# Performance work log

Measured on AMD Instinct MI355X. Metric: run time of the kernel, lower is better.

Reference implementation:

```python
import jax, jax.numpy as jnp
import numpy as np

NCLASSES = 21
CONF_THRESH = 0.5
IOU_THRESH = 0.45
TOP_K = 200
NMS_MAX_OUT = 400
NEG = jnp.float32(-1e9)  # sentinel for suppressed / below-threshold scores

B, N_BOXES = 8, 8732
LAST = NCLASSES + 4 * (NCLASSES - 1) + 1  # 102


def setup_inputs() -> dict:
    key = jax.random.key(0)
    kc, kxy, kwh, ke = jax.random.split(key, 4)
    conf = jax.random.uniform(kc, (B, N_BOXES, NCLASSES), dtype=jnp.float32)
    # plausible normalized boxes: xmin,ymin in [0,0.8], width/height in [0.01,0.2]
    xy = jax.random.uniform(kxy, (B, N_BOXES, NCLASSES - 1, 2), minval=0.0, maxval=0.8)
    wh = jax.random.uniform(kwh, (B, N_BOXES, NCLASSES - 1, 2), minval=0.01, maxval=0.2)
    boxes = jnp.concatenate([xy, xy + wh], axis=-1).reshape(B, N_BOXES, 4 * (NCLASSES - 1))
    extra = jax.random.uniform(ke, (B, N_BOXES, 1), dtype=jnp.float32)
    y_pred = jnp.concatenate([conf, boxes, extra], axis=-1)  # [B, N, 102]
    return {"y_pred": y_pred}


def _iou_one_vs_all(box, boxes):
    # box: [4] (xmin,ymin,xmax,ymax); boxes: [N,4]
    x1 = jnp.maximum(box[0], boxes[:, 0])
    y1 = jnp.maximum(box[1], boxes[:, 1])
    x2 = jnp.minimum(box[2], boxes[:, 2])
    y2 = jnp.minimum(box[3], boxes[:, 3])
    inter = jnp.maximum(x2 - x1, 0.0) * jnp.maximum(y2 - y1, 0.0)
    area_a = (box[2] - box[0]) * (box[3] - box[1])
    area_b = (boxes[:, 2] - boxes[:, 0]) * (boxes[:, 3] - boxes[:, 1])
    union = area_a + area_b - inter
    return jnp.where(union > 0.0, inter / union, 0.0)


def _nms_one_class(rows):
    # rows: [N, 7] = (class_id, conf, xmin, ymin, xmax, ymax, extra)
    n = rows.shape[0]
    scores0 = jnp.where(rows[:, 1] > CONF_THRESH, rows[:, 1], NEG)
    boxes = rows[:, 2:6]
    idx_range = jnp.arange(n)

    def step(live, _):
        best = jnp.argmax(live)
        valid = live[best] > NEG * 0.5  # any real score passed the threshold
        ious = _iou_one_vs_all(boxes[best], boxes)
        suppress = valid & ((ious > IOU_THRESH) | (idx_range == best))
        live = jnp.where(suppress, NEG, live)
        return live, (best, valid)

    _, (sel, selv) = jax.lax.scan(step, scores0, None, length=NMS_MAX_OUT)
    # gather selected rows; zero-pad invalid slots (matches tf.pad with 0)
    out = jnp.where(selv[:, None], rows[sel], 0.0)  # [NMS_MAX_OUT, 7]
    return out


def _per_image(item):
    # item: [N, 102]
    n = item.shape[0]
    conf = item[:, 1:NCLASSES]                                  # [N, C-1]
    boxes = item[:, NCLASSES:NCLASSES + 4 * (NCLASSES - 1)].reshape(n, NCLASSES - 1, 4)
    extra = item[:, -1]                                         # [N]
    class_ids = jnp.arange(1, NCLASSES, dtype=item.dtype)       # [C-1]
    rows = jnp.concatenate([
        jnp.broadcast_to(class_ids[:, None, None], (NCLASSES - 1, n, 1)),
        conf.T[:, :, None],
        jnp.transpose(boxes, (1, 0, 2)),
        jnp.broadcast_to(extra[None, :, None], (NCLASSES - 1, n, 1)),
    ], axis=-1)                                                 # [C-1, N, 7]
    per_class = jax.vmap(_nms_one_class)(rows)                  # [C-1, MAX_OUT, 7]
    filtered = per_class.reshape(-1, 7)                         # [(C-1)*MAX_OUT, 7]
    _, top_idx = jax.lax.top_k(filtered[:, 1], TOP_K)           # sorted descending
    return filtered[top_idx]                                    # [TOP_K, 7]


def reference(y_pred):
    return jax.vmap(_per_image)(y_pred)  # [B, TOP_K, 7]
```

## Files before the change

kernel.cpp:

```cpp
#include <hip/hip_runtime.h>
#include <cstdint>

#define NB 8
#define NBOX 8732
#define NCL 21
#define NCM1 20
#define LASTD 102
#define CONF_TH 0.5f
#define IOU_TH 0.45f
#define TOPK 200
#define MAXOUT 400
#define SELCAP 200
#define EMITN 256
#define NTASK (NB * NCM1)
#define THREADS 1024
#define NW 16
#define NIT 9
#define NBIN 2048
#define KPAD 8768
#define NBATCH (KPAD / 64)
#define NTR 1024
#define KPAD_TR (NTR + 64)
#define NBATCH_TR (KPAD_TR / 64)
#define CPAD 8736

#define MIDD ((double)IOU_TH + 0x1p-26)


struct SM {
    float4 selbox[SELCAP];
    float selA[SELCAP];
    uint64_t selkey[SELCAP];
    uint64_t keys[KPAD];
    uint64_t smask[2][64];
    unsigned long long extC[2];
    int hist[NBIN];
    int binstart[NBIN];
    int wavetot[NW];
    int Mshare, MtrShare, nselshare, prevNshare, doneflag;
};

__device__ __forceinline__ int iou_sup(float4 a, float aA, float4 b, float bA) {
    float x1 = fmaxf(a.x, b.x), y1 = fmaxf(a.y, b.y);
    float x2 = fminf(a.z, b.z), y2 = fminf(a.w, b.w);
    float iw = fmaxf(__fsub_rn(x2, x1), 0.0f);
    float ih = fmaxf(__fsub_rn(y2, y1), 0.0f);
    float inter = __fmul_rn(iw, ih);
    float uni = __fsub_rn(__fadd_rn(aA, bA), inter);
    return (double)inter > MIDD * (double)uni;
}

__device__ __forceinline__ float4 load_box(const float* __restrict__ img,
                                           int boxoff, uint64_t key) {
    if ((key >> 32) == 0) return make_float4(0.f, 0.f, 0.f, 0.f);
    uint32_t i = 0xFFFFFFFFu - (uint32_t)key;
    const float* bp = img + (size_t)i * LASTD + boxoff;
    return make_float4(bp[0], bp[1], bp[2], bp[3]);
}

__device__ __forceinline__ float box_area(float4 b) {
    return __fmul_rn(__fsub_rn(b.z, b.x), __fsub_rn(b.w, b.y));
}

__device__ __forceinline__ float4 shfl_box(float4 b, int c) {
    float4 r;
    r.x = __shfl(b.x, c); r.y = __shfl(b.y, c);
    r.z = __shfl(b.z, c); r.w = __shfl(b.w, c);
    return r;
}

__device__ __forceinline__ uint64_t shfl_xor_u64(uint64_t v, int m) {
    return (uint64_t)__shfl_xor((unsigned long long)v, m, 64);
}

__global__ __launch_bounds__(256) void transpose_conf(const float* __restrict__ yp,
                                                      float* __restrict__ confT,
                                                      float* __restrict__ extraT) {
    const uint32_t TOT4 = (uint32_t)NB * NBOX * LASTD / 4u;
    for (uint32_t i4 = blockIdx.x * blockDim.x + threadIdx.x; i4 < TOT4;
         i4 += gridDim.x * blockDim.x) {
        float4 v = ((const float4*)yp)[i4];
        uint32_t base = i4 * 4u;
        #pragma unroll
        for (int k = 0; k < 4; ++k) {
            uint32_t flat = base + k;
            uint32_t b = flat / (NBOX * LASTD);
            uint32_t rem = flat - b * (NBOX * LASTD);
            uint32_t row = rem / LASTD;
            uint32_t col = rem - row * LASTD;
            float f = (k == 0) ? v.x : (k == 1) ? v.y : (k == 2) ? v.z : v.w;
            if (col - 1u < (uint32_t)NCM1)
                confT[((size_t)b * NCM1 + (col - 1u)) * CPAD + row] = f;
            else if (col == LASTD - 1)
                extraT[(size_t)b * CPAD + row] = f;
        }
    }
}

template <bool TRM>
__device__ void build_keys_impl(const float* __restrict__ confsrc, int cstride,
                                SM& sm, int tid, int lane, int wav,
                                int& M, int& Mtr) {
    constexpr int PADT = TRM ? KPAD_TR : KPAD;
    float confs[NIT];
    #pragma unroll
    for (int it = 0; it < NIT; ++it) {
        int idx = it * THREADS + tid;
        confs[it] = (idx < NBOX) ? confsrc[(size_t)idx * cstride] : 0.0f;
    }
    sm.hist[tid] = 0; sm.hist[tid + THREADS] = 0;
    if (tid == 0) sm.MtrShare = 0;
    __syncthreads();

    #pragma unroll
    for (int it = 0; it < NIT; ++it) {
        int idx = it * THREADS + tid;
        if (idx < NBOX && confs[it] > CONF_TH) {
            int bin = (int)((__float_as_uint(confs[it]) - 0x3F000000u) >> 12);
            atomicAdd(&sm.hist[bin], 1);
        }
    }
    __syncthreads();

    int h0 = sm.hist[2 * tid], h1 = sm.hist[2 * tid + 1];
    int x = h0 + h1;
    int s = x;
    #pragma unroll
    for (int d = 1; d <= 32; d <<= 1) {
        int y = __shfl_down(s, d);
        if (lane + d < 64) s += y;
    }
    if (lane == 0) sm.wavetot[wav] = s;
    __syncthreads();
    int cross = 0;
    #pragma unroll
    for (int w = 0; w < NW; ++w)
        if (w > wav) cross += sm.wavetot[w];
    int Safter = cross + s - x;
    sm.binstart[2 * tid + 1] = Safter;
    sm.binstart[2 * tid] = Safter + h1;
    if (tid == 0) sm.Mshare = cross + s;
    if (TRM) {
        int cand = 0;
        if (Safter < NTR && h1 > 0) cand = Safter + h1;
        int bs0 = Safter + h1;
        if (bs0 < NTR && h0 > 0) { int c2 = bs0 + h0; cand = cand > c2 ? cand : c2; }
        if (cand > 0) atomicMax(&sm.MtrShare, cand);
    }
    sm.hist[2 * tid] = 0; sm.hist[2 * tid + 1] = 0;
    __syncthreads();
    M = sm.Mshare;
    Mtr = TRM ? sm.MtrShare : M;

    #pragma unroll
    for (int it = 0; it < NIT; ++it) {
        int idx = it * THREADS + tid;
        if (idx < NBOX && confs[it] > CONF_TH) {
            uint32_t bits = __float_as_uint(confs[it]);
            int bin = (int)((bits - 0x3F000000u) >> 12);
            if (!TRM || sm.binstart[bin] < NTR) {
                int slot = sm.binstart[bin] + atomicAdd(&sm.hist[bin], 1);
                if (!TRM || slot < PADT)
                    sm.keys[slot] = ((uint64_t)bits << 32) |
                                    (uint32_t)(0xFFFFFFFFu - (uint32_t)idx);
            }
        }
    }
    __syncthreads();
    int Mp = Mtr < PADT ? Mtr : PADT;
    for (int m = Mp + tid; m < PADT; m += THREADS) sm.keys[m] = 0;
    for (int f = tid; f < NBIN; f += THREADS) {
        int s0 = sm.binstart[f], h = sm.hist[f];
        if (TRM && (s0 >= NTR || s0 + h > PADT)) continue;
        for (int i2 = 1; i2 < h; ++i2) {
            uint64_t key = sm.keys[s0 + i2];
            int j = i2 - 1;
            while (j >= 0 && sm.keys[s0 + j] < key) {
                sm.keys[s0 + j + 1] = sm.keys[s0 + j];
                --j;
            }
            sm.keys[s0 + j + 1] = key;
        }
    }
    __syncthreads();
}

template <int KPADT, int NBATCHT>
__device__ int greedy_scan(const float* __restrict__ img, int boxoff, SM& sm,
                           int tid, int lane, int wav) {
    uint64_t keyC = sm.keys[lane];
    uint64_t keyN = sm.keys[64 + lane];
    float4 boxC = load_box(img, boxoff, keyC);
    float4 boxN = load_box(img, boxoff, keyN);
    float aC = box_area(boxC), aN = box_area(boxN);
    #pragma unroll
    for (int tt = 0; tt < 4; ++tt) {
        int c = wav + tt * NW;
        float4 cb = shfl_box(boxC, c);
        float ca = __shfl(aC, c);
        uint64_t row = 0;
        if (ca > 0.0f)
            row = __ballot(lane < c && iou_sup(cb, ca, boxC, aC));
        if (lane == 0) sm.smask[0][c] = row;
    }
    if (tid == 0) { sm.extC[0] = 0ull; sm.extC[1] = 0ull; }
    __syncthreads();

    int nsel = 0, prevN = 0;
    bool done = false;
    for (int i = 0; i < NBATCHT && !done; ++i) {
        const int p = i & 1;
        const bool vC = (keyC >> 32) != 0;
        {
            int sup = 0;
            for (int j = prevN + wav; j < nsel; j += NW)
                sup |= iou_sup(boxC, aC, sm.selbox[j], sm.selA[j]);
            unsigned long long bal = __ballot(vC && sup);
            if (lane == 0 && bal) atomicOr(&sm.extC[p], bal);
        }
        int f0 = (i + 2) * 64;
        uint64_t key2 = (f0 < KPADT) ? sm.keys[f0 + lane] : 0;
        float4 box2 = load_box(img, boxoff, key2);
        float a2 = box_area(box2);
        __syncthreads();
        const int nselPre = nsel;
        if (wav == 0) {
            unsigned long long V = __ballot(vC);
            unsigned long long E = sm.extC[p];
            if (lane == 0) sm.extC[p] = 0ull;
            uint64_t smc = sm.smask[p][lane];
            uint64_t alive = ~(E | ~V);
            uint64_t accm = 0;
            int cnt = nsel;
            while (alive && cnt < SELCAP) {
                int t = __ffsll((unsigned long long)alive) - 1;
                uint64_t bit = 1ull << t;
                accm |= bit;
                cnt++;
                unsigned long long kill = __ballot((smc >> t) & 1ull);
                alive &= ~(kill | bit);
            }
            if ((accm >> lane) & 1ull) {
                int pos = nsel + __popcll(accm & ((1ull << lane) - 1ull));
                sm.selbox[pos] = boxC;
                sm.selA[pos] = aC;
                sm.selkey[pos] = keyC;
            }
            if (lane == 0) {
                sm.nselshare = cnt;
                sm.prevNshare = nsel;
                sm.doneflag = (cnt >= SELCAP) || (V != ~0ull);
            }
        } else {
            float4 cb[5];
            float ca[5];
            unsigned amask = 0;
            #pragma unroll
            for (int k = 0; k < 5; ++k) {
                int c = (wav - 1) + k * (NW - 1);
                float4 t4 = make_float4(0.f, 0.f, 0.f, 0.f);
                float tA = 0.0f;
                if (c < 64) {
                    t4 = shfl_box(boxN, c);
                    tA = __shfl(aN, c);
                }
                cb[k] = t4; ca[k] = tA;
                if (c < 64 && tA > 0.0f) amask |= 1u << k;
            }
            unsigned long long sb = 0;
            for (int j0 = 0; j0 < nselPre && amask; j0 += 64) {
                int j = j0 + lane;
                bool jv = j < nselPre;
                float4 sbx = sm.selbox[jv ? j : 0];
                float sA = sm.selA[jv ? j : 0];
                #pragma unroll
                for (int k = 0; k < 5; ++k) {
                    if (!((amask >> k) & 1u)) continue;
                    int hit = jv && iou_sup(cb[k], ca[k], sbx, sA);
                    if (__ballot(hit)) {
                        amask &= ~(1u << k);
                        sb |= 1ull << ((wav - 1) + k * (NW - 1));
                    }
                }
            }
            #pragma unroll
            for (int k = 0; k < 5; ++k) {
                if (!((amask >> k) & 1u)) continue;
                int c = (wav - 1) + k * (NW - 1);
                uint64_t row = __ballot(lane < c && iou_sup(cb[k], ca[k], boxN, aN));
                if (lane == 0) sm.smask[p ^ 1][c] = row;
            }
            if (lane == 0 && sb) atomicOr(&sm.extC[p ^ 1], sb);
        }
        __syncthreads();
        nsel = sm.nselshare;
        prevN = sm.prevNshare;
        done = sm.doneflag != 0;
        keyC = keyN; boxC = boxN; aC = aN;
        keyN = key2; boxN = box2; aN = a2;
    }
    return nsel;
}

__device__ void emit_rows(const float* __restrict__ extrasrc, int estride,
                          int cm1, SM& sm, int nsel, float* __restrict__ rows,
                          int task, int tid) {
    float* out0 = rows + (size_t)task * MAXOUT * 7;
    for (int r = tid; r < EMITN; r += THREADS) {
        float* o = out0 + (size_t)r * 7;
        if (r < nsel) {
            uint64_t key = sm.selkey[r];
            uint32_t i = 0xFFFFFFFFu - (uint32_t)key;
            float4 bx = sm.selbox[r];
            o[0] = (float)(cm1 + 1);
            o[1] = __uint_as_float((uint32_t)(key >> 32));
            o[2] = bx.x;
            o[3] = bx.y;
            o[4] = bx.z;
            o[5] = bx.w;
            o[6] = extrasrc[(size_t)i * estride];
        } else {
            #pragma unroll
            for (int q = 0; q < 7; ++q) o[q] = 0.0f;
        }
    }
}

__global__ __launch_bounds__(THREADS) void nms_fast(const float* __restrict__ yp,
                                                    const float* __restrict__ confT,
                                                    const float* __restrict__ extraT,
                                                    float* __restrict__ rows) {
    __shared__ SM sm;
    const int task = blockIdx.x;
    const int b = task / NCM1;
    const int cm1 = task % NCM1;
    const int tid = threadIdx.x;
    const int lane = tid & 63;
    const int wav = tid >> 6;
    const float* img = yp + (size_t)b * NBOX * LASTD;
    const float* conf = confT + (size_t)task * CPAD;
    const int boxoff = NCL + 4 * cm1;

    int M, Mtr;
    build_keys_impl<true>(conf, 1, sm, tid, lane, wav, M, Mtr);
    int nsel = -1;
    if (Mtr <= KPAD_TR) {
        nsel = greedy_scan<KPAD_TR, NBATCH_TR>(img, boxoff, sm, tid, lane, wav);
        if (nsel < SELCAP && Mtr < M) nsel = -1;
    }
    if (nsel < 0) {
        build_keys_impl<false>(conf, 1, sm, tid, lane, wav, M, Mtr);
        nsel = greedy_scan<KPAD, NBATCH>(img, boxoff, sm, tid, lane, wav);
    }
    emit_rows(extraT + (size_t)b * CPAD, 1, cm1, sm, nsel, rows, task, tid);
}

__global__ __launch_bounds__(THREADS) void nms_mono(const float* __restrict__ yp,
                                                    float* __restrict__ rows) {
    __shared__ SM sm;
    const int task = blockIdx.x;
    const int b = task / NCM1;
    const int cm1 = task % NCM1;
    const int tid = threadIdx.x;
    const float* img = yp + (size_t)b * NBOX * LASTD;
    int M, Mtr;
    build_keys_impl<false>(img + 1 + cm1, LASTD, sm, tid, tid & 63, tid >> 6,
                           M, Mtr);
    int nsel = greedy_scan<KPAD, NBATCH>(img, NCL + 4 * cm1, sm, tid,
                                         tid & 63, tid >> 6);
    emit_rows(img + (LASTD - 1), LASTD, cm1, sm, nsel, rows, task, tid);
}

__global__ __launch_bounds__(THREADS) void topk_per_image(const float* __restrict__ rows,
                                                          float* __restrict__ out) {
    __shared__ uint64_t K[8192];
    const int b = blockIdx.x;
    const int tid = threadIdx.x;
    const float* rb = rows + (size_t)b * (NCM1 * MAXOUT) * 7;

    for (int xx = tid; xx < 8192; xx += THREADS) {
        int list = xx >> 8, r = xx & 255;
        uint64_t k = 0;
        if (list < NCM1) {
            int flat = list * MAXOUT + r;
            float conf = rb[(size_t)flat * 7 + 1];
            k = ((uint64_t)__float_as_uint(conf) << 32) |
                (uint32_t)(0xFFFFFFFFu - (uint32_t)flat);
        }
        K[xx] = k;
    }
    __syncthreads();

    for (int round = 0; round < 5; ++round) {
        int npairs = 16 >> round;
        int sep = 256 << round;
        for (int w = tid; w < npairs * 256; w += THREADS) {
            int p = w >> 8, t = w & 255;
            int A = p * 2 * sep;
            uint64_t a = K[A + t];
            uint64_t c = K[A + sep + 255 - t];
            K[A + t] = a > c ? a : c;
        }
        __syncthreads();
        for (int j = 128; j >= 64; j >>= 1) {
            for (int w = tid; w < npairs * 128; w += THREADS) {
                int p = w >> 7, q = w & 127;
                int t = ((q & ~(j - 1)) << 1) | (q & (j - 1));
                int A = p * 2 * sep;
                uint64_t x0 = K[A + t];
                uint64_t x1 = K[A + t + j];
                if (x0 < x1) { K[A + t] = x1; K[A + t + j] = x0; }
            }
            __syncthreads();
        }
        for (int w = tid; w < npairs * 256; w += THREADS) {
            int p = w >> 8, t = w & 255;
            int xI = p * 2 * sep + t;
            uint64_t v = K[xI];
            #pragma unroll
            for (int j = 32; j >= 1; j >>= 1) {
                uint64_t pr = shfl_xor_u64(v, j);
                uint64_t mx = v > pr ? v : pr;
                uint64_t mn = v > pr ? pr : v;
                v = ((t & j) == 0) ? mx : mn;
            }
            K[xI] = v;
        }
        __syncthreads();
    }

    if (tid < TOPK) {
        uint64_t key = K[tid];
        uint32_t flat = 0xFFFFFFFFu - (uint32_t)key;
        const float* src = rb + (size_t)flat * 7;
        float* o = out + ((size_t)b * TOPK + tid) * 7;
        #pragma unroll
        for (int q = 0; q < 7; ++q) o[q] = src[q];
    }
}

extern "C" void kernel_launch(void* const* d_in, const int* in_sizes, int n_in,
                              void* d_out, int out_size, void* d_ws, size_t ws_size,
                              hipStream_t stream) {
    const float* yp = (const float*)d_in[0];
    float* rows = (float*)d_ws;
    const size_t rowsB = (size_t)NTASK * MAXOUT * 7 * sizeof(float);
    float* confT = (float*)((char*)d_ws + rowsB);
    const size_t confB = (size_t)NTASK * CPAD * sizeof(float);
    float* extraT = (float*)((char*)confT + confB);
    const size_t extraB = (size_t)NB * CPAD * sizeof(float);
    const size_t need = rowsB + confB + extraB;
    float* out = (float*)d_out;

    if (ws_size >= need) {
        hipLaunchKernelGGL(transpose_conf, dim3(2048), dim3(256), 0, stream,
                           yp, confT, extraT);
        hipLaunchKernelGGL(nms_fast, dim3(NTASK), dim3(THREADS), 0, stream,
                           yp, confT, extraT, rows);
    } else {
        hipLaunchKernelGGL(nms_mono, dim3(NTASK), dim3(THREADS), 0, stream,
                           yp, rows);
    }
    hipLaunchKernelGGL(topk_per_image, dim3(NB), dim3(THREADS), 0, stream,
                       rows, out);
}
```

Measured before the change: 59.34 us.

## Replace truncated greedy NMS scan with precomputed suppression bitmask matrix

The fast path now keeps only the top ~512-576 candidates. It precomputes a pairwise IoU suppression bitmask matrix in shared memory, built with wave ballots, and then runs the greedy selection as a single-wave bitmask sweep. This replaces the previous batched greedy scan over up to 1088 keys. The aim is to cut serialized per-selection IoU work and block-wide syncs. In exchange it uses a smaller truncation window, which may send more tasks down the full fallback path, and it spends extra shared memory on a union layout.

```diff
diff --git a/kernel.cpp b/kernel.cpp
--- a/kernel.cpp
+++ b/kernel.cpp
@@ -19,9 +19,9 @@
 #define NBIN 2048
 #define KPAD 8768
 #define NBATCH (KPAD / 64)
-#define NTR 1024
-#define KPAD_TR (NTR + 64)
-#define NBATCH_TR (KPAD_TR / 64)
+#define NTR 512
+#define NMX 576
+#define NWORD 9
 #define CPAD 8736
 
 #define MIDD ((double)IOU_TH + 0x1p-26)
@@ -38,6 +38,18 @@
     int binstart[NBIN];
     int wavetot[NW];
     int Mshare, MtrShare, nselshare, prevNshare, doneflag;
+};
+
+struct FastSM {
+    uint64_t keys[NMX];
+    uint64_t M[NMX][NWORD];
+    float4 bx[NMX];
+    float ar[NMX];
+    int acc[SELCAP];
+    int hist[NBIN];
+    int binstart[NBIN];
+    int wavetot[NW];
+    int Mshare, MtrShare, nselshare;
 };
 
 __device__ __forceinline__ int iou_sup(float4 a, float aA, float4 b, float bA) {
@@ -97,11 +109,10 @@
     }
 }
 
-template <bool TRM>
+template <class SMT, bool TRM, int PADT, int NTRT>
 __device__ void build_keys_impl(const float* __restrict__ confsrc, int cstride,
-                                SM& sm, int tid, int lane, int wav,
+                                SMT& sm, int tid, int lane, int wav,
                                 int& M, int& Mtr) {
-    constexpr int PADT = TRM ? KPAD_TR : KPAD;
     float confs[NIT];
     #pragma unroll
     for (int it = 0; it < NIT; ++it) {
@@ -142,9 +153,9 @@
     if (tid == 0) sm.Mshare = cross + s;
     if (TRM) {
         int cand = 0;
-        if (Safter < NTR && h1 > 0) cand = Safter + h1;
+        if (Safter < NTRT && h1 > 0) cand = Safter + h1;
         int bs0 = Safter + h1;
-        if (bs0 < NTR && h0 > 0) { int c2 = bs0 + h0; cand = cand > c2 ? cand : c2; }
+        if (bs0 < NTRT && h0 > 0) { int c2 = bs0 + h0; cand = cand > c2 ? cand : c2; }
         if (cand > 0) atomicMax(&sm.MtrShare, cand);
     }
     sm.hist[2 * tid] = 0; sm.hist[2 * tid + 1] = 0;
@@ -158,7 +169,7 @@
         if (idx < NBOX && confs[it] > CONF_TH) {
             uint32_t bits = __float_as_uint(confs[it]);
             int bin = (int)((bits - 0x3F000000u) >> 12);
-            if (!TRM || sm.binstart[bin] < NTR) {
+            if (!TRM || sm.binstart[bin] < NTRT) {
                 int slot = sm.binstart[bin] + atomicAdd(&sm.hist[bin], 1);
                 if (!TRM || slot < PADT)
                     sm.keys[slot] = ((uint64_t)bits << 32) |
@@ -171,7 +182,7 @@
     for (int m = Mp + tid; m < PADT; m += THREADS) sm.keys[m] = 0;
     for (int f = tid; f < NBIN; f += THREADS) {
         int s0 = sm.binstart[f], h = sm.hist[f];
-        if (TRM && (s0 >= NTR || s0 + h > PADT)) continue;
+        if (TRM && (s0 >= NTRT || s0 + h > PADT)) continue;
         for (int i2 = 1; i2 < h; ++i2) {
             uint64_t key = sm.keys[s0 + i2];
             int j = i2 - 1;
@@ -330,7 +341,7 @@
                                                     const float* __restrict__ confT,
                                                     const float* __restrict__ extraT,
                                                     float* __restrict__ rows) {
-    __shared__ SM sm;
+    __shared__ union USM { SM full; FastSM fast; } u;
     const int task = blockIdx.x;
     const int b = task / NCM1;
     const int cm1 = task % NCM1;
@@ -342,17 +353,93 @@
     const int boxoff = NCL + 4 * cm1;
 
     int M, Mtr;
-    build_keys_impl<true>(conf, 1, sm, tid, lane, wav, M, Mtr);
+    build_keys_impl<FastSM, true, NMX, NTR>(conf, 1, u.fast, tid, lane, wav,
+                                            M, Mtr);
     int nsel = -1;
-    if (Mtr <= KPAD_TR) {
-        nsel = greedy_scan<KPAD_TR, NBATCH_TR>(img, boxoff, sm, tid, lane, wav);
+    if (Mtr <= NMX) {
+        for (int c = tid; c < NMX; c += THREADS) {
+            float4 bb = load_box(img, boxoff, u.fast.keys[c]);
+            u.fast.bx[c] = bb;
+            u.fast.ar[c] = box_area(bb);
+        }
+        __syncthreads();
+        for (int k = 0; k < NMX / NW; ++k) {
+            int a = wav + k * NW;
+            float4 ab = u.fast.bx[a];
+            float aa = u.fast.ar[a];
+            if (aa > 0.0f) {
+                for (int w = a >> 6; w < NWORD; ++w) {
+                    int bc = w * 64 + lane;
+                    int hit = (bc > a) &&
+                              iou_sup(ab, aa, u.fast.bx[bc], u.fast.ar[bc]);
+                    unsigned long long bal = __ballot(hit);
+                    if (lane == 0) u.fast.M[a][w] = bal;
+                }
+            } else {
+                for (int w = a >> 6; w < NWORD; ++w)
+                    if (lane == 0) u.fast.M[a][w] = 0ull;
+            }
+        }
+        __syncthreads();
+        if (wav == 0) {
+            uint64_t alive = 0;
+            if (lane < NWORD) {
+                int rem = Mtr - lane * 64;
+                alive = (rem >= 64) ? ~0ull
+                      : (rem > 0 ? ((1ull << rem) - 1ull) : 0ull);
+            }
+            int cnt = 0;
+            for (int w = 0; w < NWORD && cnt < SELCAP; ++w) {
+                uint64_t cur = (uint64_t)__shfl((unsigned long long)alive, w);
+                while (cur && cnt < SELCAP) {
+                    int t = __ffsll((unsigned long long)cur) - 1;
+                    int c = w * 64 + t;
+                    if (lane == 0) u.fast.acc[cnt] = c;
+                    cnt++;
+                    uint64_t row = (lane < NWORD) ? u.fast.M[c][lane] : 0ull;
+                    alive &= ~row;
+                    uint64_t roww = (uint64_t)__shfl((unsigned long long)row, w);
+                    cur &= ~(roww | (1ull << t));
+                }
+            }
+            if (lane == 0) u.fast.nselshare = cnt;
+        }
+        __syncthreads();
+        nsel = u.fast.nselshare;
         if (nsel < SELCAP && Mtr < M) nsel = -1;
+        if (nsel >= 0) {
+            const float* extrasrc = extraT + (size_t)b * CPAD;
+            float* out0 = rows + (size_t)task * MAXOUT * 7;
+            for (int r = tid; r < EMITN; r += THREADS) {
+                float* o = out0 + (size_t)r * 7;
+                if (r < nsel) {
+                    int c = u.fast.acc[r];
+                    uint64_t key = u.fast.keys[c];
+                    uint32_t i = 0xFFFFFFFFu - (uint32_t)key;
+                    float4 bxv = u.fast.bx[c];
+                    o[0] = (float)(cm1 + 1);
+                    o[1] = __uint_as_float((uint32_t)(key >> 32));
+                    o[2] = bxv.x;
+                    o[3] = bxv.y;
+                    o[4] = bxv.z;
+                    o[5] = bxv.w;
+                    o[6] = extrasrc[i];
+                } else {
+                    #pragma unroll
+                    for (int q = 0; q < 7; ++q) o[q] = 0.0f;
+                }
+            }
+        }
     }
     if (nsel < 0) {
-        build_keys_impl<false>(conf, 1, sm, tid, lane, wav, M, Mtr);
-        nsel = greedy_scan<KPAD, NBATCH>(img, boxoff, sm, tid, lane, wav);
-    }
-    emit_rows(extraT + (size_t)b * CPAD, 1, cm1, sm, nsel, rows, task, tid);
+        __syncthreads();
+        int M2, Mt2;
+        build_keys_impl<SM, false, KPAD, 0>(conf, 1, u.full, tid, lane, wav,
+                                            M2, Mt2);
+        int ns2 = greedy_scan<KPAD, NBATCH>(img, boxoff, u.full, tid, lane, wav);
+        emit_rows(extraT + (size_t)b * CPAD, 1, cm1, u.full, ns2, rows, task,
+                  tid);
+    }
 }
 
 __global__ __launch_bounds__(THREADS) void nms_mono(const float* __restrict__ yp,
@@ -364,8 +451,8 @@
     const int tid = threadIdx.x;
     const float* img = yp + (size_t)b * NBOX * LASTD;
     int M, Mtr;
-    build_keys_impl<false>(img + 1 + cm1, LASTD, sm, tid, tid & 63, tid >> 6,
-                           M, Mtr);
+    build_keys_impl<SM, false, KPAD, 0>(img + 1 + cm1, LASTD, sm, tid,
+                                        tid & 63, tid >> 6, M, Mtr);
     int nsel = greedy_scan<KPAD, NBATCH>(img, NCL + 4 * cm1, sm, tid,
                                          tid & 63, tid >> 6);
     emit_rows(img + (LASTD - 1), LASTD, cm1, sm, nsel, rows, task, tid);
```

Measured after the change: 103.5 us. 1.74x slower.

## Stage conf transpose through shared-memory tiles and shrink NTR candidate threshold

Applied to the files above, without the earlier changes.

The conf/extra transpose now works in 64-row tiles per block. Each block stages the needed columns in LDS and then writes confT and extraT coalesced along the row dimension, replacing the scattered strided global stores. Separately, NTR drops from 1024 to 512 and KPAD_TR is padded by 128 instead of 64, which changes the truncated-candidate path of NMS. The retuned NTR may raise fallback frequency if more candidates are needed.

```diff
diff --git a/kernel.cpp b/kernel.cpp
--- a/kernel.cpp
+++ b/kernel.cpp
@@ -19,10 +19,14 @@
 #define NBIN 2048
 #define KPAD 8768
 #define NBATCH (KPAD / 64)
-#define NTR 1024
-#define KPAD_TR (NTR + 64)
+#define NTR 512
+#define KPAD_TR (NTR + 128)
 #define NBATCH_TR (KPAD_TR / 64)
 #define CPAD 8736
+#define TROWS 64
+#define NTILE ((NBOX + TROWS - 1) / TROWS)
+#define TSLOT 21
+#define TPITCH 68
 
 #define MIDD ((double)IOU_TH + 0x1p-26)
 
@@ -76,23 +80,41 @@
 __global__ __launch_bounds__(256) void transpose_conf(const float* __restrict__ yp,
                                                       float* __restrict__ confT,
                                                       float* __restrict__ extraT) {
-    const uint32_t TOT4 = (uint32_t)NB * NBOX * LASTD / 4u;
-    for (uint32_t i4 = blockIdx.x * blockDim.x + threadIdx.x; i4 < TOT4;
-         i4 += gridDim.x * blockDim.x) {
-        float4 v = ((const float4*)yp)[i4];
-        uint32_t base = i4 * 4u;
+    __shared__ float tile[TSLOT * TPITCH];
+    const int blk = blockIdx.x;
+    const int b = blk / NTILE;
+    const int t0 = blk - b * NTILE;
+    const int r0 = t0 * TROWS;
+    const int nrow = (NBOX - r0) < TROWS ? (NBOX - r0) : TROWS;
+    const int nflat4 = nrow * LASTD / 4;
+    const float4* src = (const float4*)(yp + ((size_t)b * NBOX + r0) * LASTD);
+
+    for (int i4 = threadIdx.x; i4 < nflat4; i4 += 256) {
+        float4 v = src[i4];
+        int base = i4 * 4;
         #pragma unroll
         for (int k = 0; k < 4; ++k) {
-            uint32_t flat = base + k;
-            uint32_t b = flat / (NBOX * LASTD);
-            uint32_t rem = flat - b * (NBOX * LASTD);
-            uint32_t row = rem / LASTD;
-            uint32_t col = rem - row * LASTD;
-            float f = (k == 0) ? v.x : (k == 1) ? v.y : (k == 2) ? v.z : v.w;
-            if (col - 1u < (uint32_t)NCM1)
-                confT[((size_t)b * NCM1 + (col - 1u)) * CPAD + row] = f;
-            else if (col == LASTD - 1)
-                extraT[(size_t)b * CPAD + row] = f;
+            int f = base + k;
+            int row = f / LASTD;
+            int col = f - row * LASTD;
+            float val = (k == 0) ? v.x : (k == 1) ? v.y : (k == 2) ? v.z : v.w;
+            int slot = -1;
+            if ((unsigned)(col - 1) < (unsigned)NCM1) slot = col - 1;
+            else if (col == LASTD - 1) slot = NCM1;
+            if (slot >= 0) tile[slot * TPITCH + row] = val;
+        }
+    }
+    __syncthreads();
+
+    for (int w = threadIdx.x; w < TSLOT * TROWS; w += 256) {
+        int slot = w >> 6, ro = w & 63;
+        int row = r0 + ro;
+        if (ro < nrow) {
+            float v = tile[slot * TPITCH + ro];
+            if (slot < NCM1)
+                confT[((size_t)b * NCM1 + slot) * CPAD + row] = v;
+            else
+                extraT[(size_t)b * CPAD + row] = v;
         }
     }
 }
@@ -453,8 +475,8 @@
     float* out = (float*)d_out;
 
     if (ws_size >= need) {
-        hipLaunchKernelGGL(transpose_conf, dim3(2048), dim3(256), 0, stream,
-                           yp, confT, extraT);
+        hipLaunchKernelGGL(transpose_conf, dim3(NB * NTILE), dim3(256), 0,
+                           stream, yp, confT, extraT);
         hipLaunchKernelGGL(nms_fast, dim3(NTASK), dim3(THREADS), 0, stream,
                            yp, confT, extraT, rows);
     } else {
```

New measurement: 55.90 us. 5.8% less time.
